# Performance work log

Measured on AMD Instinct MI355X. Metric: run time of the kernel, lower is better.

Reference implementation:

```python
import jax, jax.numpy as jnp
import numpy as np

D_MODEL = 512
NUM_HEADS = 8
D_K = D_MODEL // NUM_HEADS


def _linear(x, w, b):
    # torch nn.Linear: y = x @ w.T + b, w: [out, in]
    return jnp.einsum('bsd,ed->bse', x, w) + b


def _attn_proj(x, w1, b1, w2, b2):
    return jax.nn.silu(_linear(x, w1, b1)) * _linear(x, w2, b2)


def setup_inputs() -> dict:
    key = jax.random.key(0)
    ks = jax.random.split(key, 20)
    B, S, D = 4, 8192, D_MODEL
    scale = 1.0 / np.sqrt(D)
    inp = {
        'query': jax.random.normal(ks[0], (B, S, D), jnp.float32),
        'key': jax.random.normal(ks[1], (B, S, D), jnp.float32),
        'value': jax.random.normal(ks[2], (B, S, D), jnp.float32),
    }
    names = ['q_w1', 'q_w2', 'k_w1', 'k_w2', 'v_w1', 'v_w2', 'out_w']
    for i, n in enumerate(names):
        inp[n] = jax.random.normal(ks[3 + i], (D, D), jnp.float32) * scale
    bnames = ['q_b1', 'q_b2', 'k_b1', 'k_b2', 'v_b1', 'v_b2', 'out_b']
    for i, n in enumerate(bnames):
        inp[n] = jax.random.normal(ks[10 + i], (D,), jnp.float32) * 0.01
    return inp


def reference(query, key, value,
              q_w1, q_w2, k_w1, k_w2, v_w1, v_w2, out_w,
              q_b1, q_b2, k_b1, k_b2, v_b1, v_b2, out_b):
    B = query.shape[0]
    eps = 1e-6
    # projections -> [B, H, S, d_k]
    def split_heads(x):
        return x.reshape(B, -1, NUM_HEADS, D_K).transpose(0, 2, 1, 3)
    q = split_heads(_attn_proj(query, q_w1, q_b1, q_w2, q_b2))
    k = split_heads(_attn_proj(key, k_w1, k_b1, k_w2, k_b2))
    v = split_heads(_attn_proj(value, v_w1, v_b1, v_w2, v_b2))

    phi_q = jax.nn.elu(q) + 1.0
    phi_k = jax.nn.elu(k) + 1.0
    # key_value: [B, H, d_k, d_k]
    key_value = jnp.einsum('bhsd,bhse->bhde', phi_k, v)
    key_sum = phi_k.sum(axis=-2)                       # [B, H, d_k]
    qk_sum = jnp.einsum('bhsd,bhd->bhs', phi_q, key_sum)
    numerator = jnp.einsum('bhsd,bhde->bhse', phi_q, key_value)
    attn = numerator / (qk_sum[..., None] + eps)       # [B, H, S, d_k]

    x = attn.transpose(0, 2, 1, 3).reshape(B, -1, NUM_HEADS * D_K)
    return _linear(x, out_w, out_b)
```

## Files before the change

### kernel.cpp

```cpp
#include <hip/hip_runtime.h>
#include <stdint.h>


#define DMODEL 512
#define NHEAD 8
#define BATCH 4
#define SEQ 8192
#define BSROWS (BATCH * SEQ)
#define NSPLIT 16
#define CHUNK (SEQ / NSPLIT)

typedef __attribute__((ext_vector_type(8))) short short8;
typedef __attribute__((ext_vector_type(4))) short short4v;
typedef __attribute__((ext_vector_type(4))) float f32x4;
typedef __attribute__((ext_vector_type(4))) unsigned short ushort4v;

__device__ __forceinline__ unsigned short f2bf(float f) {
  union { float f; uint32_t u; } v; v.f = f;
  uint32_t u = v.u;
  u += 0x7fffu + ((u >> 16) & 1u);
  return (unsigned short)(u >> 16);
}
__device__ __forceinline__ float bf2f(unsigned short h) {
  union { float f; uint32_t u; } v; v.u = ((uint32_t)h) << 16; return v.f;
}
__device__ __forceinline__ f32x4 zero4() {
  f32x4 z; z[0] = 0.f; z[1] = 0.f; z[2] = 0.f; z[3] = 0.f; return z;
}
__device__ __forceinline__ void gload_lds16(const unsigned short* g, unsigned short* l) {
  __builtin_amdgcn_global_load_lds((const __attribute__((address_space(1))) void*)g,
                                   (__attribute__((address_space(3))) void*)l, 16, 0, 0);
}

struct WPtrs { const float* w[7]; };

__global__ void convert_weights_kernel(WPtrs wp, unsigned short* __restrict__ wbf) {
  int gid = blockIdx.x * 256 + threadIdx.x;
  int which = gid >> 16;
  int rem = gid & 65535;
  float4 v = ((const float4*)wp.w[which])[rem];
  ushort4v o;
  o[0] = f2bf(v.x); o[1] = f2bf(v.y); o[2] = f2bf(v.z); o[3] = f2bf(v.w);
  *(ushort4v*)(wbf + (size_t)which * 262144 + (size_t)rem * 4) = o;
}

__global__ void convert_x_kernel(const float* __restrict__ q, const float* __restrict__ k,
                                 const float* __restrict__ v, unsigned short* __restrict__ xbf) {
  size_t t = (size_t)blockIdx.x * 256 + threadIdx.x;
  int which = (int)(t >> 21);
  size_t rem = t & 2097151;
  const float* src = which == 0 ? q : (which == 1 ? k : v);
  const float4* s4 = (const float4*)src + rem * 2;
  float4 a = s4[0], b = s4[1];
  short8 o;
  o[0] = (short)f2bf(a.x); o[1] = (short)f2bf(a.y);
  o[2] = (short)f2bf(a.z); o[3] = (short)f2bf(a.w);
  o[4] = (short)f2bf(b.x); o[5] = (short)f2bf(b.y);
  o[6] = (short)f2bf(b.z); o[7] = (short)f2bf(b.w);
  *(short8*)(xbf + ((size_t)which << 24) + rem * 8) = o;
}

struct ProjArgs {
  const float* b1[3];
  const float* b2[3];
  unsigned short* out[3];
};

__global__ __launch_bounds__(512, 2) void proj_kernel(ProjArgs pa,
                                                      const unsigned short* __restrict__ wbf,
                                                      const unsigned short* __restrict__ xbf) {
  const int which = blockIdx.y;
  const unsigned short* __restrict__ x = xbf + ((size_t)which << 24);
  const unsigned short* __restrict__ w1 = wbf + (size_t)which * 524288;
  const unsigned short* __restrict__ w2 = w1 + 262144;
  const float* __restrict__ b1p = pa.b1[which];
  const float* __restrict__ b2p = pa.b2[which];
  unsigned short* __restrict__ outp = pa.out[which];
  const bool PHI = (which < 2);

  const int mt = blockIdx.x >> 2, nt = blockIdx.x & 3;
  const int m0 = mt * 256, n0 = nt * 128;
  const int tid = threadIdx.x;
  const int wave = tid >> 6, lane = tid & 63;
  const int lrow = lane & 15, quad = lane >> 4;
  const int m_off = (wave >> 1) * 64, n_off = (wave & 1) * 64;

  __shared__ unsigned short lds[2 * 32768];

  const int srow_l = lane >> 3;
  const int kq_l = (lane & 7) ^ srow_l;
  const int swz = lrow & 7;

  f32x4 acc1[4][4], acc2[4][4];
#pragma unroll
  for (int i = 0; i < 4; i++)
#pragma unroll
    for (int j = 0; j < 4; j++) { acc1[i][j] = zero4(); acc2[i][j] = zero4(); }

  {
#pragma unroll
    for (int i = 0; i < 4; i++) {
      int ig = wave * 4 + i;
      gload_lds16(x + (size_t)(m0 + ig * 8 + srow_l) * 512 + kq_l * 8,
                  lds + ig * 512);
    }
#pragma unroll
    for (int j = 0; j < 2; j++) {
      int igb = wave * 2 + j;
      size_t roff = (size_t)(n0 + igb * 8 + srow_l) * 512 + kq_l * 8;
      gload_lds16(w1 + roff, lds + 16384 + igb * 512);
      gload_lds16(w2 + roff, lds + 24576 + igb * 512);
    }
  }

  for (int t = 0; t < 8; ++t) {
    unsigned short* cur = lds + (t & 1) * 32768;
    if (t < 7) {
      unsigned short* nxt = lds + ((t + 1) & 1) * 32768;
      const int k0 = (t + 1) * 64;
#pragma unroll
      for (int i = 0; i < 4; i++) {
        int ig = wave * 4 + i;
        gload_lds16(x + (size_t)(m0 + ig * 8 + srow_l) * 512 + k0 + kq_l * 8,
                    nxt + ig * 512);
      }
#pragma unroll
      for (int j = 0; j < 2; j++) {
        int igb = wave * 2 + j;
        size_t roff = (size_t)(n0 + igb * 8 + srow_l) * 512 + k0 + kq_l * 8;
        gload_lds16(w1 + roff, nxt + 16384 + igb * 512);
        gload_lds16(w2 + roff, nxt + 24576 + igb * 512);
      }
      asm volatile("s_waitcnt vmcnt(8)" ::: "memory");
    } else {
      asm volatile("s_waitcnt vmcnt(0)" ::: "memory");
    }
    __builtin_amdgcn_s_barrier();

#pragma unroll
    for (int kk = 0; kk < 64; kk += 32) {
      const int e8 = (kk >> 3) + quad;
      short8 af[4], b1f[4], b2f[4];
#pragma unroll
      for (int mi = 0; mi < 4; mi++)
        af[mi] = *(const short8*)(cur + (m_off + mi * 16 + lrow) * 64 + ((e8 ^ swz) << 3));
#pragma unroll
      for (int ni = 0; ni < 4; ni++) {
        int rr = n_off + ni * 16 + lrow;
        b1f[ni] = *(const short8*)(cur + 16384 + rr * 64 + ((e8 ^ swz) << 3));
        b2f[ni] = *(const short8*)(cur + 24576 + rr * 64 + ((e8 ^ swz) << 3));
      }
#pragma unroll
      for (int ni = 0; ni < 4; ni++)
#pragma unroll
        for (int mi = 0; mi < 4; mi++) {
          acc1[mi][ni] = __builtin_amdgcn_mfma_f32_16x16x32_bf16(af[mi], b1f[ni], acc1[mi][ni], 0, 0, 0);
          acc2[mi][ni] = __builtin_amdgcn_mfma_f32_16x16x32_bf16(af[mi], b2f[ni], acc2[mi][ni], 0, 0, 0);
        }
    }
    __builtin_amdgcn_s_barrier();
  }

  if (which == 0) {
#pragma unroll
    for (int ni = 0; ni < 4; ni++) {
      int n = n0 + n_off + ni * 16 + lrow;
      float bb1 = b1p[n], bb2 = b2p[n];
#pragma unroll
      for (int mi = 0; mi < 4; mi++)
#pragma unroll
        for (int r = 0; r < 4; r++) {
          int m = m0 + m_off + mi * 16 + quad * 4 + r;
          float v1 = acc1[mi][ni][r] + bb1;
          float v2 = acc2[mi][ni][r] + bb2;
          float y = v1 * (1.f / (1.f + __expf(-v1))) * v2;
          y = (y > 0.f) ? (y + 1.f) : __expf(y);
          outp[(size_t)m * 512 + n] = f2bf(y);
        }
    }
  } else {
    const int bI = m0 >> 13;
    const int sb = (m0 & 8191) + m_off + quad * 4;
#pragma unroll
    for (int ni = 0; ni < 4; ni++) {
      int n = n0 + n_off + ni * 16 + lrow;
      float bb1 = b1p[n], bb2 = b2p[n];
      int h = n >> 6, d = n & 63;
      unsigned short* dst0 = outp + (((size_t)bI * 8 + h) * 64 + d) * 8192 + sb;
#pragma unroll
      for (int mi = 0; mi < 4; mi++) {
        short4v o;
#pragma unroll
        for (int r = 0; r < 4; r++) {
          float v1 = acc1[mi][ni][r] + bb1;
          float v2 = acc2[mi][ni][r] + bb2;
          float y = v1 * (1.f / (1.f + __expf(-v1))) * v2;
          if (PHI) y = (y > 0.f) ? (y + 1.f) : __expf(y);
          o[r] = (short)f2bf(y);
        }
        *(short4v*)(dst0 + mi * 16) = o;
      }
    }
  }
}

__global__ __launch_bounds__(256) void kv_kernel(const unsigned short* __restrict__ kT,
                                                 const unsigned short* __restrict__ vT,
                                                 float* __restrict__ kvt_part,
                                                 float* __restrict__ ksum_part) {
  const int chunk = blockIdx.x & (NSPLIT - 1);
  const int bh = blockIdx.x >> 4;
  const int tid = threadIdx.x;
  const int wave = tid >> 6, lane = tid & 63;
  const int lrow = lane & 15, quad = lane >> 4;

  __shared__ float ls_acc[4096];
  __shared__ float ls_ksum[64];
  if (tid < 64) ls_ksum[tid] = 0.f;
#pragma unroll
  for (int i = 0; i < 16; i++) ls_acc[tid + 256 * i] = 0.f;

  const unsigned short* vrow = vT + (size_t)bh * 64 * 8192;
  const unsigned short* krow = kT + (size_t)bh * 64 * 8192;
  const int s_w = chunk * CHUNK + wave * 128;

  short8 ones;
#pragma unroll
  for (int j = 0; j < 8; j++) ones[j] = (short)0x3F80;

  f32x4 acc[4][4], aks[4];
#pragma unroll
  for (int i = 0; i < 4; i++) {
    aks[i] = zero4();
#pragma unroll
    for (int j = 0; j < 4; j++) acc[i][j] = zero4();
  }

  for (int it = 0; it < 4; it++) {
    const int s0 = s_w + it * 32 + quad * 8;
    short8 af[4], bfr[4];
#pragma unroll
    for (int mi = 0; mi < 4; mi++)
      af[mi] = *(const short8*)(vrow + (size_t)(mi * 16 + lrow) * 8192 + s0);
#pragma unroll
    for (int ni = 0; ni < 4; ni++)
      bfr[ni] = *(const short8*)(krow + (size_t)(ni * 16 + lrow) * 8192 + s0);
#pragma unroll
    for (int ni = 0; ni < 4; ni++) {
      aks[ni] = __builtin_amdgcn_mfma_f32_16x16x32_bf16(ones, bfr[ni], aks[ni], 0, 0, 0);
#pragma unroll
      for (int mi = 0; mi < 4; mi++)
        acc[mi][ni] = __builtin_amdgcn_mfma_f32_16x16x32_bf16(af[mi], bfr[ni], acc[mi][ni], 0, 0, 0);
    }
  }

  __syncthreads();
#pragma unroll
  for (int mi = 0; mi < 4; mi++)
#pragma unroll
    for (int ni = 0; ni < 4; ni++)
#pragma unroll
      for (int r = 0; r < 4; r++)
        atomicAdd(&ls_acc[(mi * 16 + quad * 4 + r) * 64 + ni * 16 + lrow], acc[mi][ni][r]);
  if (quad == 0) {
#pragma unroll
    for (int ni = 0; ni < 4; ni++) atomicAdd(&ls_ksum[ni * 16 + lrow], aks[ni][0]);
  }
  __syncthreads();

  float* op = kvt_part + ((size_t)chunk * 32 + bh) * 4096;
#pragma unroll
  for (int i = 0; i < 16; i++) op[tid + 256 * i] = ls_acc[tid + 256 * i];
  if (tid < 64) ksum_part[((size_t)chunk * 32 + bh) * 64 + tid] = ls_ksum[tid];
}

__global__ void kv_reduce_kernel(const float* __restrict__ kvt_part,
                                 const float* __restrict__ ksum_part,
                                 unsigned short* __restrict__ kvT,
                                 unsigned short* __restrict__ ksum_bf) {
  const int bh = blockIdx.x >> 2, seg = blockIdx.x & 3;
  const int idx = seg * 1024 + threadIdx.x * 4;
  float4 s = make_float4(0.f, 0.f, 0.f, 0.f);
#pragma unroll
  for (int c = 0; c < NSPLIT; c++) {
    float4 v = *(const float4*)&kvt_part[((size_t)c * 32 + bh) * 4096 + idx];
    s.x += v.x; s.y += v.y; s.z += v.z; s.w += v.w;
  }
  ushort4v o;
  o[0] = f2bf(s.x); o[1] = f2bf(s.y); o[2] = f2bf(s.z); o[3] = f2bf(s.w);
  *(ushort4v*)(kvT + (size_t)bh * 4096 + idx) = o;
  if (seg == 0 && threadIdx.x < 64) {
    float t = 0.f;
#pragma unroll
    for (int c = 0; c < NSPLIT; c++) t += ksum_part[((size_t)c * 32 + bh) * 64 + threadIdx.x];
    ksum_bf[bh * 64 + threadIdx.x] = f2bf(t);
  }
}

__global__ __launch_bounds__(256) void attn_kernel(const unsigned short* __restrict__ phiQ,
                                                   const unsigned short* __restrict__ kvT,
                                                   const unsigned short* __restrict__ ksum_bf,
                                                   unsigned short* __restrict__ xattn) {
  const int bh = blockIdx.x & 31;
  const int st = blockIdx.x >> 5;
  const int b = bh >> 3, h = bh & 7;
  const int tid = threadIdx.x;
  const int wave = tid >> 6, lane = tid & 63;
  const int lrow = lane & 15, quad = lane >> 4;
  const size_t rowbase = (size_t)b * SEQ + st * 128 + wave * 32;

  f32x4 acc[2][4], aqs[2];
#pragma unroll
  for (int i = 0; i < 2; i++) {
    aqs[i] = zero4();
#pragma unroll
    for (int j = 0; j < 4; j++) acc[i][j] = zero4();
  }

#pragma unroll
  for (int kk = 0; kk < 64; kk += 32) {
    short8 ks = *(const short8*)(ksum_bf + bh * 64 + kk + quad * 8);
    short8 af[2];
#pragma unroll
    for (int mi = 0; mi < 2; mi++)
      af[mi] = *(const short8*)(phiQ + (rowbase + mi * 16 + lrow) * 512 + h * 64 + kk + quad * 8);
#pragma unroll
    for (int mi = 0; mi < 2; mi++)
      aqs[mi] = __builtin_amdgcn_mfma_f32_16x16x32_bf16(af[mi], ks, aqs[mi], 0, 0, 0);
#pragma unroll
    for (int ni = 0; ni < 4; ni++) {
      short8 bfr = *(const short8*)(kvT + (size_t)bh * 4096 + (ni * 16 + lrow) * 64 + kk + quad * 8);
#pragma unroll
      for (int mi = 0; mi < 2; mi++)
        acc[mi][ni] = __builtin_amdgcn_mfma_f32_16x16x32_bf16(af[mi], bfr, acc[mi][ni], 0, 0, 0);
    }
  }
#pragma unroll
  for (int mi = 0; mi < 2; mi++) {
#pragma unroll
    for (int r = 0; r < 4; r++) {
      float inv = 1.f / (aqs[mi][r] + 1e-6f);
      size_t m = rowbase + mi * 16 + quad * 4 + r;
#pragma unroll
      for (int ni = 0; ni < 4; ni++)
        xattn[m * 512 + h * 64 + ni * 16 + lrow] = f2bf(acc[mi][ni][r] * inv);
    }
  }
}

__global__ __launch_bounds__(512, 2) void out_gemm_kernel(const unsigned short* __restrict__ xattn,
                                                          const unsigned short* __restrict__ wo,
                                                          const float* __restrict__ ob,
                                                          float* __restrict__ out) {
  const int mt = blockIdx.x >> 2, nt = blockIdx.x & 3;
  const int m0 = mt * 256, n0 = nt * 128;
  const int tid = threadIdx.x;
  const int wave = tid >> 6, lane = tid & 63;
  const int lrow = lane & 15, quad = lane >> 4;
  const int m_off = (wave >> 1) * 64, n_off = (wave & 1) * 64;

  __shared__ unsigned short lds[2 * 24576];

  const int srow_l = lane >> 3;
  const int kq_l = (lane & 7) ^ srow_l;
  const int swz = lrow & 7;

  f32x4 acc[4][4];
#pragma unroll
  for (int i = 0; i < 4; i++)
#pragma unroll
    for (int j = 0; j < 4; j++) acc[i][j] = zero4();

  {
#pragma unroll
    for (int i = 0; i < 4; i++) {
      int ig = wave * 4 + i;
      gload_lds16(xattn + (size_t)(m0 + ig * 8 + srow_l) * 512 + kq_l * 8,
                  lds + ig * 512);
    }
#pragma unroll
    for (int j = 0; j < 2; j++) {
      int igb = wave * 2 + j;
      gload_lds16(wo + (size_t)(n0 + igb * 8 + srow_l) * 512 + kq_l * 8,
                  lds + 16384 + igb * 512);
    }
  }

  for (int t = 0; t < 8; ++t) {
    unsigned short* cur = lds + (t & 1) * 24576;
    if (t < 7) {
      unsigned short* nxt = lds + ((t + 1) & 1) * 24576;
      const int k0 = (t + 1) * 64;
#pragma unroll
      for (int i = 0; i < 4; i++) {
        int ig = wave * 4 + i;
        gload_lds16(xattn + (size_t)(m0 + ig * 8 + srow_l) * 512 + k0 + kq_l * 8,
                    nxt + ig * 512);
      }
#pragma unroll
      for (int j = 0; j < 2; j++) {
        int igb = wave * 2 + j;
        gload_lds16(wo + (size_t)(n0 + igb * 8 + srow_l) * 512 + k0 + kq_l * 8,
                    nxt + 16384 + igb * 512);
      }
      asm volatile("s_waitcnt vmcnt(6)" ::: "memory");
    } else {
      asm volatile("s_waitcnt vmcnt(0)" ::: "memory");
    }
    __builtin_amdgcn_s_barrier();

#pragma unroll
    for (int kk = 0; kk < 64; kk += 32) {
      const int e8 = (kk >> 3) + quad;
      short8 af[4], bfr[4];
#pragma unroll
      for (int mi = 0; mi < 4; mi++)
        af[mi] = *(const short8*)(cur + (m_off + mi * 16 + lrow) * 64 + ((e8 ^ swz) << 3));
#pragma unroll
      for (int ni = 0; ni < 4; ni++)
        bfr[ni] = *(const short8*)(cur + 16384 + (n_off + ni * 16 + lrow) * 64 + ((e8 ^ swz) << 3));
#pragma unroll
      for (int ni = 0; ni < 4; ni++)
#pragma unroll
        for (int mi = 0; mi < 4; mi++)
          acc[mi][ni] = __builtin_amdgcn_mfma_f32_16x16x32_bf16(af[mi], bfr[ni], acc[mi][ni], 0, 0, 0);
    }
    __builtin_amdgcn_s_barrier();
  }

#pragma unroll
  for (int ni = 0; ni < 4; ni++) {
    int n = n0 + n_off + ni * 16 + lrow;
    float bb = ob[n];
#pragma unroll
    for (int mi = 0; mi < 4; mi++)
#pragma unroll
      for (int r = 0; r < 4; r++) {
        int m = m0 + m_off + mi * 16 + quad * 4 + r;
        out[(size_t)m * 512 + n] = acc[mi][ni][r] + bb;
      }
  }
}

extern "C" void kernel_launch(void* const* d_in, const int* in_sizes, int n_in,
                              void* d_out, int out_size, void* d_ws, size_t ws_size,
                              hipStream_t stream) {
  char* ws = (char*)d_ws;
  size_t off = 0;
  auto alloc = [&](size_t bytes) -> void* {
    void* p = ws + off;
    off += (bytes + 255) & ~(size_t)255;
    return p;
  };
  unsigned short* wbf = (unsigned short*)alloc((size_t)7 * 262144 * 2);
  unsigned short* phiQ = (unsigned short*)alloc((size_t)BSROWS * 512 * 2);
  unsigned short* kT = (unsigned short*)alloc((size_t)BSROWS * 512 * 2);
  unsigned short* vT = (unsigned short*)alloc((size_t)BSROWS * 512 * 2);
  unsigned short* xbf = (unsigned short*)alloc((size_t)3 * BSROWS * 512 * 2);
  if (off > ws_size) return;

  char* xr = (char*)xbf;
  unsigned short* xattn = (unsigned short*)xr;
  float* kvt_part = (float*)(xr + 67108864);
  float* ksum_part = (float*)(xr + 75497472);
  unsigned short* kvT = (unsigned short*)(xr + 75628544);
  unsigned short* ksum_bf = (unsigned short*)(xr + 75890688);

  WPtrs wp;
  for (int i = 0; i < 7; i++) wp.w[i] = (const float*)d_in[3 + i];
  convert_weights_kernel<<<1792, 256, 0, stream>>>(wp, wbf);
  convert_x_kernel<<<24576, 256, 0, stream>>>((const float*)d_in[0], (const float*)d_in[1],
                                              (const float*)d_in[2], xbf);

  ProjArgs pa;
  pa.b1[0] = (const float*)d_in[10]; pa.b2[0] = (const float*)d_in[11];
  pa.b1[1] = (const float*)d_in[12]; pa.b2[1] = (const float*)d_in[13];
  pa.b1[2] = (const float*)d_in[14]; pa.b2[2] = (const float*)d_in[15];
  pa.out[0] = phiQ; pa.out[1] = kT; pa.out[2] = vT;
  proj_kernel<<<dim3(512, 3), 512, 0, stream>>>(pa, wbf, xbf);

  kv_kernel<<<512, 256, 0, stream>>>(kT, vT, kvt_part, ksum_part);
  kv_reduce_kernel<<<128, 256, 0, stream>>>(kvt_part, ksum_part, kvT, ksum_bf);
  attn_kernel<<<2048, 256, 0, stream>>>(phiQ, kvT, ksum_bf, xattn);
  out_gemm_kernel<<<512, 512, 0, stream>>>(xattn, wbf + (size_t)6 * 262144,
                                           (const float*)d_in[16], (float*)d_out);
}
```

Before: 485.7 us.

## Interleave LDS reads and MFMA phases with priority and remap GEMM block order

Rewrites the main loops of the projection and output GEMMs into several barrier-separated phases. Each phase loads a subset of fragments from LDS, waits on lgkmcnt, and runs an MFMA burst under s_setprio(1). The next tile's global->LDS prefetch is issued early and drained with vmcnt(0) only at the end of the tile, so the waves stay staggered and LDS traffic overlaps matrix work. Block indices are also remapped so consecutive blocks are spread across the M dimension in groups of 8, aiming for better cache or XCD locality. In exchange, each tile now has many more barriers, which may add synchronization overhead.

```diff
diff --git a/kernel.cpp b/kernel.cpp
--- a/kernel.cpp
+++ b/kernel.cpp
@@ -78,7 +78,8 @@
   unsigned short* __restrict__ outp = pa.out[which];
   const bool PHI = (which < 2);
 
-  const int mt = blockIdx.x >> 2, nt = blockIdx.x & 3;
+  const int wg = (blockIdx.x & 7) * 64 + (blockIdx.x >> 3);
+  const int mt = wg >> 2, nt = wg & 3;
   const int m0 = mt * 256, n0 = nt * 128;
   const int tid = threadIdx.x;
   const int wave = tid >> 6, lane = tid & 63;
@@ -97,67 +98,109 @@
 #pragma unroll
     for (int j = 0; j < 4; j++) { acc1[i][j] = zero4(); acc2[i][j] = zero4(); }
 
-  {
+  auto stage = [&](unsigned short* dst, int k0) {
 #pragma unroll
     for (int i = 0; i < 4; i++) {
       int ig = wave * 4 + i;
-      gload_lds16(x + (size_t)(m0 + ig * 8 + srow_l) * 512 + kq_l * 8,
-                  lds + ig * 512);
+      gload_lds16(x + (size_t)(m0 + ig * 8 + srow_l) * 512 + k0 + kq_l * 8,
+                  dst + ig * 512);
     }
 #pragma unroll
     for (int j = 0; j < 2; j++) {
       int igb = wave * 2 + j;
-      size_t roff = (size_t)(n0 + igb * 8 + srow_l) * 512 + kq_l * 8;
-      gload_lds16(w1 + roff, lds + 16384 + igb * 512);
-      gload_lds16(w2 + roff, lds + 24576 + igb * 512);
-    }
-  }
+      size_t roff = (size_t)(n0 + igb * 8 + srow_l) * 512 + k0 + kq_l * 8;
+      gload_lds16(w1 + roff, dst + 16384 + igb * 512);
+      gload_lds16(w2 + roff, dst + 24576 + igb * 512);
+    }
+  };
+
+  stage(lds, 0);
+  asm volatile("s_waitcnt vmcnt(0)" ::: "memory");
+  __builtin_amdgcn_s_barrier();
 
   for (int t = 0; t < 8; ++t) {
     unsigned short* cur = lds + (t & 1) * 32768;
-    if (t < 7) {
-      unsigned short* nxt = lds + ((t + 1) & 1) * 32768;
-      const int k0 = (t + 1) * 64;
-#pragma unroll
-      for (int i = 0; i < 4; i++) {
-        int ig = wave * 4 + i;
-        gload_lds16(x + (size_t)(m0 + ig * 8 + srow_l) * 512 + k0 + kq_l * 8,
-                    nxt + ig * 512);
-      }
-#pragma unroll
-      for (int j = 0; j < 2; j++) {
-        int igb = wave * 2 + j;
-        size_t roff = (size_t)(n0 + igb * 8 + srow_l) * 512 + k0 + kq_l * 8;
-        gload_lds16(w1 + roff, nxt + 16384 + igb * 512);
-        gload_lds16(w2 + roff, nxt + 24576 + igb * 512);
-      }
-      asm volatile("s_waitcnt vmcnt(8)" ::: "memory");
-    } else {
-      asm volatile("s_waitcnt vmcnt(0)" ::: "memory");
-    }
-    __builtin_amdgcn_s_barrier();
-
-#pragma unroll
-    for (int kk = 0; kk < 64; kk += 32) {
-      const int e8 = (kk >> 3) + quad;
-      short8 af[4], b1f[4], b2f[4];
+    unsigned short* nxt = lds + ((t + 1) & 1) * 32768;
+    short8 af[4], b1f[4], b2f[4];
+
+    {
+      const int e8 = quad;
 #pragma unroll
       for (int mi = 0; mi < 4; mi++)
         af[mi] = *(const short8*)(cur + (m_off + mi * 16 + lrow) * 64 + ((e8 ^ swz) << 3));
 #pragma unroll
-      for (int ni = 0; ni < 4; ni++) {
-        int rr = n_off + ni * 16 + lrow;
-        b1f[ni] = *(const short8*)(cur + 16384 + rr * 64 + ((e8 ^ swz) << 3));
-        b2f[ni] = *(const short8*)(cur + 24576 + rr * 64 + ((e8 ^ swz) << 3));
-      }
-#pragma unroll
       for (int ni = 0; ni < 4; ni++)
-#pragma unroll
-        for (int mi = 0; mi < 4; mi++) {
-          acc1[mi][ni] = __builtin_amdgcn_mfma_f32_16x16x32_bf16(af[mi], b1f[ni], acc1[mi][ni], 0, 0, 0);
-          acc2[mi][ni] = __builtin_amdgcn_mfma_f32_16x16x32_bf16(af[mi], b2f[ni], acc2[mi][ni], 0, 0, 0);
-        }
-    }
+        b1f[ni] = *(const short8*)(cur + 16384 + (n_off + ni * 16 + lrow) * 64 + ((e8 ^ swz) << 3));
+    }
+    if (t < 7) stage(nxt, (t + 1) * 64);
+    __builtin_amdgcn_s_barrier();
+    asm volatile("s_waitcnt lgkmcnt(0)" ::: "memory");
+    __builtin_amdgcn_sched_barrier(0);
+    __builtin_amdgcn_s_setprio(1);
+#pragma unroll
+    for (int ni = 0; ni < 4; ni++)
+#pragma unroll
+      for (int mi = 0; mi < 4; mi++)
+        acc1[mi][ni] = __builtin_amdgcn_mfma_f32_16x16x32_bf16(af[mi], b1f[ni], acc1[mi][ni], 0, 0, 0);
+    __builtin_amdgcn_s_setprio(0);
+    __builtin_amdgcn_s_barrier();
+
+    {
+      const int e8 = quad;
+#pragma unroll
+      for (int ni = 0; ni < 4; ni++)
+        b2f[ni] = *(const short8*)(cur + 24576 + (n_off + ni * 16 + lrow) * 64 + ((e8 ^ swz) << 3));
+    }
+    __builtin_amdgcn_s_barrier();
+    asm volatile("s_waitcnt lgkmcnt(0)" ::: "memory");
+    __builtin_amdgcn_sched_barrier(0);
+    __builtin_amdgcn_s_setprio(1);
+#pragma unroll
+    for (int ni = 0; ni < 4; ni++)
+#pragma unroll
+      for (int mi = 0; mi < 4; mi++)
+        acc2[mi][ni] = __builtin_amdgcn_mfma_f32_16x16x32_bf16(af[mi], b2f[ni], acc2[mi][ni], 0, 0, 0);
+    __builtin_amdgcn_s_setprio(0);
+    __builtin_amdgcn_s_barrier();
+
+    {
+      const int e8 = 4 + quad;
+#pragma unroll
+      for (int mi = 0; mi < 4; mi++)
+        af[mi] = *(const short8*)(cur + (m_off + mi * 16 + lrow) * 64 + ((e8 ^ swz) << 3));
+#pragma unroll
+      for (int ni = 0; ni < 4; ni++)
+        b1f[ni] = *(const short8*)(cur + 16384 + (n_off + ni * 16 + lrow) * 64 + ((e8 ^ swz) << 3));
+    }
+    __builtin_amdgcn_s_barrier();
+    asm volatile("s_waitcnt lgkmcnt(0)" ::: "memory");
+    __builtin_amdgcn_sched_barrier(0);
+    __builtin_amdgcn_s_setprio(1);
+#pragma unroll
+    for (int ni = 0; ni < 4; ni++)
+#pragma unroll
+      for (int mi = 0; mi < 4; mi++)
+        acc1[mi][ni] = __builtin_amdgcn_mfma_f32_16x16x32_bf16(af[mi], b1f[ni], acc1[mi][ni], 0, 0, 0);
+    __builtin_amdgcn_s_setprio(0);
+    __builtin_amdgcn_s_barrier();
+
+    {
+      const int e8 = 4 + quad;
+#pragma unroll
+      for (int ni = 0; ni < 4; ni++)
+        b2f[ni] = *(const short8*)(cur + 24576 + (n_off + ni * 16 + lrow) * 64 + ((e8 ^ swz) << 3));
+    }
+    asm volatile("s_waitcnt vmcnt(0)" ::: "memory");
+    __builtin_amdgcn_s_barrier();
+    asm volatile("s_waitcnt lgkmcnt(0)" ::: "memory");
+    __builtin_amdgcn_sched_barrier(0);
+    __builtin_amdgcn_s_setprio(1);
+#pragma unroll
+    for (int ni = 0; ni < 4; ni++)
+#pragma unroll
+      for (int mi = 0; mi < 4; mi++)
+        acc2[mi][ni] = __builtin_amdgcn_mfma_f32_16x16x32_bf16(af[mi], b2f[ni], acc2[mi][ni], 0, 0, 0);
+    __builtin_amdgcn_s_setprio(0);
     __builtin_amdgcn_s_barrier();
   }
 
@@ -352,7 +395,8 @@
                                                           const unsigned short* __restrict__ wo,
                                                           const float* __restrict__ ob,
                                                           float* __restrict__ out) {
-  const int mt = blockIdx.x >> 2, nt = blockIdx.x & 3;
+  const int wg = (blockIdx.x & 7) * 64 + (blockIdx.x >> 3);
+  const int mt = wg >> 2, nt = wg & 3;
   const int m0 = mt * 256, n0 = nt * 128;
   const int tid = threadIdx.x;
   const int wave = tid >> 6, lane = tid & 63;
@@ -371,61 +415,67 @@
 #pragma unroll
     for (int j = 0; j < 4; j++) acc[i][j] = zero4();
 
-  {
+  auto stage = [&](unsigned short* dst, int k0) {
 #pragma unroll
     for (int i = 0; i < 4; i++) {
       int ig = wave * 4 + i;
-      gload_lds16(xattn + (size_t)(m0 + ig * 8 + srow_l) * 512 + kq_l * 8,
-                  lds + ig * 512);
+      gload_lds16(xattn + (size_t)(m0 + ig * 8 + srow_l) * 512 + k0 + kq_l * 8,
+                  dst + ig * 512);
     }
 #pragma unroll
     for (int j = 0; j < 2; j++) {
       int igb = wave * 2 + j;
-      gload_lds16(wo + (size_t)(n0 + igb * 8 + srow_l) * 512 + kq_l * 8,
-                  lds + 16384 + igb * 512);
-    }
-  }
+      gload_lds16(wo + (size_t)(n0 + igb * 8 + srow_l) * 512 + k0 + kq_l * 8,
+                  dst + 16384 + igb * 512);
+    }
+  };
+
+  stage(lds, 0);
+  asm volatile("s_waitcnt vmcnt(0)" ::: "memory");
+  __builtin_amdgcn_s_barrier();
 
   for (int t = 0; t < 8; ++t) {
     unsigned short* cur = lds + (t & 1) * 24576;
-    if (t < 7) {
-      unsigned short* nxt = lds + ((t + 1) & 1) * 24576;
-      const int k0 = (t + 1) * 64;
-#pragma unroll
-      for (int i = 0; i < 4; i++) {
-        int ig = wave * 4 + i;
-        gload_lds16(xattn + (size_t)(m0 + ig * 8 + srow_l) * 512 + k0 + kq_l * 8,
-                    nxt + ig * 512);
-      }
-#pragma unroll
-      for (int j = 0; j < 2; j++) {
-        int igb = wave * 2 + j;
-        gload_lds16(wo + (size_t)(n0 + igb * 8 + srow_l) * 512 + k0 + kq_l * 8,
-                    nxt + 16384 + igb * 512);
-      }
-      asm volatile("s_waitcnt vmcnt(6)" ::: "memory");
-    } else {
-      asm volatile("s_waitcnt vmcnt(0)" ::: "memory");
-    }
-    __builtin_amdgcn_s_barrier();
-
-#pragma unroll
-    for (int kk = 0; kk < 64; kk += 32) {
-      const int e8 = (kk >> 3) + quad;
-      short8 af[4], bfr[4];
+    unsigned short* nxt = lds + ((t + 1) & 1) * 24576;
+    short8 af[4], bfr[4];
+
+#pragma unroll
+    for (int half = 0; half < 2; half++) {
+      const int e8 = half * 4 + quad;
 #pragma unroll
       for (int mi = 0; mi < 4; mi++)
         af[mi] = *(const short8*)(cur + (m_off + mi * 16 + lrow) * 64 + ((e8 ^ swz) << 3));
 #pragma unroll
-      for (int ni = 0; ni < 4; ni++)
+      for (int ni = 0; ni < 2; ni++)
         bfr[ni] = *(const short8*)(cur + 16384 + (n_off + ni * 16 + lrow) * 64 + ((e8 ^ swz) << 3));
-#pragma unroll
-      for (int ni = 0; ni < 4; ni++)
+      if (half == 0 && t < 7) stage(nxt, (t + 1) * 64);
+      __builtin_amdgcn_s_barrier();
+      asm volatile("s_waitcnt lgkmcnt(0)" ::: "memory");
+      __builtin_amdgcn_sched_barrier(0);
+      __builtin_amdgcn_s_setprio(1);
+#pragma unroll
+      for (int ni = 0; ni < 2; ni++)
 #pragma unroll
         for (int mi = 0; mi < 4; mi++)
           acc[mi][ni] = __builtin_amdgcn_mfma_f32_16x16x32_bf16(af[mi], bfr[ni], acc[mi][ni], 0, 0, 0);
-    }
-    __builtin_amdgcn_s_barrier();
+      __builtin_amdgcn_s_setprio(0);
+      __builtin_amdgcn_s_barrier();
+#pragma unroll
+      for (int ni = 2; ni < 4; ni++)
+        bfr[ni] = *(const short8*)(cur + 16384 + (n_off + ni * 16 + lrow) * 64 + ((e8 ^ swz) << 3));
+      if (half == 1) asm volatile("s_waitcnt vmcnt(0)" ::: "memory");
+      __builtin_amdgcn_s_barrier();
+      asm volatile("s_waitcnt lgkmcnt(0)" ::: "memory");
+      __builtin_amdgcn_sched_barrier(0);
+      __builtin_amdgcn_s_setprio(1);
+#pragma unroll
+      for (int ni = 2; ni < 4; ni++)
+#pragma unroll
+        for (int mi = 0; mi < 4; mi++)
+          acc[mi][ni] = __builtin_amdgcn_mfma_f32_16x16x32_bf16(af[mi], bfr[ni], acc[mi][ni], 0, 0, 0);
+      __builtin_amdgcn_s_setprio(0);
+      __builtin_amdgcn_s_barrier();
+    }
   }
 
 #pragma unroll
```

Measured after the change: 486.3 us. No clear change (+0.1%).

## Use 16-wave workgroups for projection and output GEMMs with block swizzle

Applied to the files above, without the earlier changes.

Both GEMM kernels now run with 1024 threads (16 waves) per 256x128 tile instead of 8. Each wave covers 64x32 outputs rather than 64x64, which halves its accumulators and the per-wave staging loads, and the waitcnt values are adjusted to match. Block indices are also remapped with a stride-8 swizzle so that neighbouring workgroups handle different M tiles, which is likely aimed at spreading work across XCDs and their caches. The extra waves may hide latency better, but the A-fragment LDS reads are now duplicated across twice as many waves, and launch_bounds(1024,4) may not be achievable given 128KB of LDS per block.

```diff
diff --git a/kernel.cpp b/kernel.cpp
--- a/kernel.cpp
+++ b/kernel.cpp
@@ -66,9 +66,9 @@
   unsigned short* out[3];
 };
 
-__global__ __launch_bounds__(512, 2) void proj_kernel(ProjArgs pa,
-                                                      const unsigned short* __restrict__ wbf,
-                                                      const unsigned short* __restrict__ xbf) {
+__global__ __launch_bounds__(1024, 4) void proj_kernel(ProjArgs pa,
+                                                       const unsigned short* __restrict__ wbf,
+                                                       const unsigned short* __restrict__ xbf) {
   const int which = blockIdx.y;
   const unsigned short* __restrict__ x = xbf + ((size_t)which << 24);
   const unsigned short* __restrict__ w1 = wbf + (size_t)which * 524288;
@@ -78,12 +78,14 @@
   unsigned short* __restrict__ outp = pa.out[which];
   const bool PHI = (which < 2);
 
-  const int mt = blockIdx.x >> 2, nt = blockIdx.x & 3;
+  const int wg = (blockIdx.x & 7) * 64 + (blockIdx.x >> 3);
+  const int mt = wg >> 2, nt = wg & 3;
   const int m0 = mt * 256, n0 = nt * 128;
   const int tid = threadIdx.x;
   const int wave = tid >> 6, lane = tid & 63;
   const int lrow = lane & 15, quad = lane >> 4;
-  const int m_off = (wave >> 1) * 64, n_off = (wave & 1) * 64;
+  const int m_off = (wave >> 2) * 64;
+  const int n_off = (wave & 3) * 32;
 
   __shared__ unsigned short lds[2 * 32768];
 
@@ -91,47 +93,31 @@
   const int kq_l = (lane & 7) ^ srow_l;
   const int swz = lrow & 7;
 
-  f32x4 acc1[4][4], acc2[4][4];
+  f32x4 acc1[4][2], acc2[4][2];
 #pragma unroll
   for (int i = 0; i < 4; i++)
 #pragma unroll
-    for (int j = 0; j < 4; j++) { acc1[i][j] = zero4(); acc2[i][j] = zero4(); }
-
-  {
-#pragma unroll
-    for (int i = 0; i < 4; i++) {
-      int ig = wave * 4 + i;
-      gload_lds16(x + (size_t)(m0 + ig * 8 + srow_l) * 512 + kq_l * 8,
-                  lds + ig * 512);
-    }
-#pragma unroll
-    for (int j = 0; j < 2; j++) {
-      int igb = wave * 2 + j;
-      size_t roff = (size_t)(n0 + igb * 8 + srow_l) * 512 + kq_l * 8;
-      gload_lds16(w1 + roff, lds + 16384 + igb * 512);
-      gload_lds16(w2 + roff, lds + 24576 + igb * 512);
-    }
-  }
+    for (int j = 0; j < 2; j++) { acc1[i][j] = zero4(); acc2[i][j] = zero4(); }
+
+  auto stage = [&](unsigned short* dst, int k0) {
+#pragma unroll
+    for (int i = 0; i < 2; i++) {
+      int ig = wave * 2 + i;
+      gload_lds16(x + (size_t)(m0 + ig * 8 + srow_l) * 512 + k0 + kq_l * 8,
+                  dst + ig * 512);
+    }
+    size_t roff = (size_t)(n0 + wave * 8 + srow_l) * 512 + k0 + kq_l * 8;
+    gload_lds16(w1 + roff, dst + 16384 + wave * 512);
+    gload_lds16(w2 + roff, dst + 24576 + wave * 512);
+  };
+
+  stage(lds, 0);
 
   for (int t = 0; t < 8; ++t) {
     unsigned short* cur = lds + (t & 1) * 32768;
     if (t < 7) {
-      unsigned short* nxt = lds + ((t + 1) & 1) * 32768;
-      const int k0 = (t + 1) * 64;
-#pragma unroll
-      for (int i = 0; i < 4; i++) {
-        int ig = wave * 4 + i;
-        gload_lds16(x + (size_t)(m0 + ig * 8 + srow_l) * 512 + k0 + kq_l * 8,
-                    nxt + ig * 512);
-      }
-#pragma unroll
-      for (int j = 0; j < 2; j++) {
-        int igb = wave * 2 + j;
-        size_t roff = (size_t)(n0 + igb * 8 + srow_l) * 512 + k0 + kq_l * 8;
-        gload_lds16(w1 + roff, nxt + 16384 + igb * 512);
-        gload_lds16(w2 + roff, nxt + 24576 + igb * 512);
-      }
-      asm volatile("s_waitcnt vmcnt(8)" ::: "memory");
+      stage(lds + ((t + 1) & 1) * 32768, (t + 1) * 64);
+      asm volatile("s_waitcnt vmcnt(4)" ::: "memory");
     } else {
       asm volatile("s_waitcnt vmcnt(0)" ::: "memory");
     }
@@ -140,18 +126,18 @@
 #pragma unroll
     for (int kk = 0; kk < 64; kk += 32) {
       const int e8 = (kk >> 3) + quad;
-      short8 af[4], b1f[4], b2f[4];
+      short8 af[4], b1f[2], b2f[2];
 #pragma unroll
       for (int mi = 0; mi < 4; mi++)
         af[mi] = *(const short8*)(cur + (m_off + mi * 16 + lrow) * 64 + ((e8 ^ swz) << 3));
 #pragma unroll
-      for (int ni = 0; ni < 4; ni++) {
+      for (int ni = 0; ni < 2; ni++) {
         int rr = n_off + ni * 16 + lrow;
         b1f[ni] = *(const short8*)(cur + 16384 + rr * 64 + ((e8 ^ swz) << 3));
         b2f[ni] = *(const short8*)(cur + 24576 + rr * 64 + ((e8 ^ swz) << 3));
       }
 #pragma unroll
-      for (int ni = 0; ni < 4; ni++)
+      for (int ni = 0; ni < 2; ni++)
 #pragma unroll
         for (int mi = 0; mi < 4; mi++) {
           acc1[mi][ni] = __builtin_amdgcn_mfma_f32_16x16x32_bf16(af[mi], b1f[ni], acc1[mi][ni], 0, 0, 0);
@@ -163,7 +149,7 @@
 
   if (which == 0) {
 #pragma unroll
-    for (int ni = 0; ni < 4; ni++) {
+    for (int ni = 0; ni < 2; ni++) {
       int n = n0 + n_off + ni * 16 + lrow;
       float bb1 = b1p[n], bb2 = b2p[n];
 #pragma unroll
@@ -182,7 +168,7 @@
     const int bI = m0 >> 13;
     const int sb = (m0 & 8191) + m_off + quad * 4;
 #pragma unroll
-    for (int ni = 0; ni < 4; ni++) {
+    for (int ni = 0; ni < 2; ni++) {
       int n = n0 + n_off + ni * 16 + lrow;
       float bb1 = b1p[n], bb2 = b2p[n];
       int h = n >> 6, d = n & 63;
@@ -348,16 +334,18 @@
   }
 }
 
-__global__ __launch_bounds__(512, 2) void out_gemm_kernel(const unsigned short* __restrict__ xattn,
-                                                          const unsigned short* __restrict__ wo,
-                                                          const float* __restrict__ ob,
-                                                          float* __restrict__ out) {
-  const int mt = blockIdx.x >> 2, nt = blockIdx.x & 3;
+__global__ __launch_bounds__(1024, 4) void out_gemm_kernel(const unsigned short* __restrict__ xattn,
+                                                           const unsigned short* __restrict__ wo,
+                                                           const float* __restrict__ ob,
+                                                           float* __restrict__ out) {
+  const int wg = (blockIdx.x & 7) * 64 + (blockIdx.x >> 3);
+  const int mt = wg >> 2, nt = wg & 3;
   const int m0 = mt * 256, n0 = nt * 128;
   const int tid = threadIdx.x;
   const int wave = tid >> 6, lane = tid & 63;
   const int lrow = lane & 15, quad = lane >> 4;
-  const int m_off = (wave >> 1) * 64, n_off = (wave & 1) * 64;
+  const int m_off = (wave >> 2) * 64;
+  const int n_off = (wave & 3) * 32;
 
   __shared__ unsigned short lds[2 * 24576];
 
@@ -365,45 +353,30 @@
   const int kq_l = (lane & 7) ^ srow_l;
   const int swz = lrow & 7;
 
-  f32x4 acc[4][4];
+  f32x4 acc[4][2];
 #pragma unroll
   for (int i = 0; i < 4; i++)
 #pragma unroll
-    for (int j = 0; j < 4; j++) acc[i][j] = zero4();
-
-  {
-#pragma unroll
-    for (int i = 0; i < 4; i++) {
-      int ig = wave * 4 + i;
-      gload_lds16(xattn + (size_t)(m0 + ig * 8 + srow_l) * 512 + kq_l * 8,
-                  lds + ig * 512);
-    }
-#pragma unroll
-    for (int j = 0; j < 2; j++) {
-      int igb = wave * 2 + j;
-      gload_lds16(wo + (size_t)(n0 + igb * 8 + srow_l) * 512 + kq_l * 8,
-                  lds + 16384 + igb * 512);
-    }
-  }
+    for (int j = 0; j < 2; j++) acc[i][j] = zero4();
+
+  auto stage = [&](unsigned short* dst, int k0) {
+#pragma unroll
+    for (int i = 0; i < 2; i++) {
+      int ig = wave * 2 + i;
+      gload_lds16(xattn + (size_t)(m0 + ig * 8 + srow_l) * 512 + k0 + kq_l * 8,
+                  dst + ig * 512);
+    }
+    gload_lds16(wo + (size_t)(n0 + wave * 8 + srow_l) * 512 + k0 + kq_l * 8,
+                dst + 16384 + wave * 512);
+  };
+
+  stage(lds, 0);
 
   for (int t = 0; t < 8; ++t) {
     unsigned short* cur = lds + (t & 1) * 24576;
     if (t < 7) {
-      unsigned short* nxt = lds + ((t + 1) & 1) * 24576;
-      const int k0 = (t + 1) * 64;
-#pragma unroll
-      for (int i = 0; i < 4; i++) {
-        int ig = wave * 4 + i;
-        gload_lds16(xattn + (size_t)(m0 + ig * 8 + srow_l) * 512 + k0 + kq_l * 8,
-                    nxt + ig * 512);
-      }
-#pragma unroll
-      for (int j = 0; j < 2; j++) {
-        int igb = wave * 2 + j;
-        gload_lds16(wo + (size_t)(n0 + igb * 8 + srow_l) * 512 + k0 + kq_l * 8,
-                    nxt + 16384 + igb * 512);
-      }
-      asm volatile("s_waitcnt vmcnt(6)" ::: "memory");
+      stage(lds + ((t + 1) & 1) * 24576, (t + 1) * 64);
+      asm volatile("s_waitcnt vmcnt(3)" ::: "memory");
     } else {
       asm volatile("s_waitcnt vmcnt(0)" ::: "memory");
     }
@@ -412,15 +385,15 @@
 #pragma unroll
     for (int kk = 0; kk < 64; kk += 32) {
       const int e8 = (kk >> 3) + quad;
-      short8 af[4], bfr[4];
+      short8 af[4], bfr[2];
 #pragma unroll
       for (int mi = 0; mi < 4; mi++)
         af[mi] = *(const short8*)(cur + (m_off + mi * 16 + lrow) * 64 + ((e8 ^ swz) << 3));
 #pragma unroll
-      for (int ni = 0; ni < 4; ni++)
+      for (int ni = 0; ni < 2; ni++)
         bfr[ni] = *(const short8*)(cur + 16384 + (n_off + ni * 16 + lrow) * 64 + ((e8 ^ swz) << 3));
 #pragma unroll
-      for (int ni = 0; ni < 4; ni++)
+      for (int ni = 0; ni < 2; ni++)
 #pragma unroll
         for (int mi = 0; mi < 4; mi++)
           acc[mi][ni] = __builtin_amdgcn_mfma_f32_16x16x32_bf16(af[mi], bfr[ni], acc[mi][ni], 0, 0, 0);
@@ -429,7 +402,7 @@
   }
 
 #pragma unroll
-  for (int ni = 0; ni < 4; ni++) {
+  for (int ni = 0; ni < 2; ni++) {
     int n = n0 + n_off + ni * 16 + lrow;
     float bb = ob[n];
 #pragma unroll
@@ -477,11 +450,11 @@
   pa.b1[1] = (const float*)d_in[12]; pa.b2[1] = (const float*)d_in[13];
   pa.b1[2] = (const float*)d_in[14]; pa.b2[2] = (const float*)d_in[15];
   pa.out[0] = phiQ; pa.out[1] = kT; pa.out[2] = vT;
-  proj_kernel<<<dim3(512, 3), 512, 0, stream>>>(pa, wbf, xbf);
+  proj_kernel<<<dim3(512, 3), 1024, 0, stream>>>(pa, wbf, xbf);
 
   kv_kernel<<<512, 256, 0, stream>>>(kT, vT, kvt_part, ksum_part);
   kv_reduce_kernel<<<128, 256, 0, stream>>>(kvt_part, ksum_part, kvT, ksum_bf);
   attn_kernel<<<2048, 256, 0, stream>>>(phiQ, kvT, ksum_bf, xattn);
-  out_gemm_kernel<<<512, 512, 0, stream>>>(xattn, wbf + (size_t)6 * 262144,
-                                           (const float*)d_in[16], (float*)d_out);
-}
+  out_gemm_kernel<<<512, 1024, 0, stream>>>(xattn, wbf + (size_t)6 * 262144,
+                                            (const float*)d_in[16], (float*)d_out);
+}
```

After: 477.1 us. Within noise of the previous version (-1.8%).
